# Kernel tuning notes

Hardware: AMD Instinct MI355X
Metric: run time of the kernel (lower is better)

The kernel has to match this reference:

```python
import jax, jax.numpy as jnp
import numpy as np

M, N, EMB, H, ENC, T = 4096, 256, 64, 128, 128, 100


def _lstm_dir(x, Wih, Whh, b, h0, c0):
    # x: (T, M, E); PyTorch LSTM gate order i, f, g, o
    def step(carry, xt):
        h, c = carry
        g = xt @ Wih + h @ Whh + b
        i, f, gg, o = jnp.split(g, 4, axis=-1)
        c = jax.nn.sigmoid(f) * c + jax.nn.sigmoid(i) * jnp.tanh(gg)
        h = jax.nn.sigmoid(o) * jnp.tanh(c)
        return (h, c), h
    _, hs = jax.lax.scan(step, (h0, c0), x)
    return hs  # (T, M, H)


def setup_inputs() -> dict:
    key = jax.random.key(0)
    ks = jax.random.split(key, 14)
    rn = lambda k, sh, s: jax.random.normal(k, sh, jnp.float32) * s
    return {
        "lane_features": jax.random.normal(ks[0], (M, 600), jnp.float32),
        "obs_encoding": jax.random.normal(ks[1], (N, 128), jnp.float32),
        "embed_W": rn(ks[2], (4, EMB), 0.5),
        "embed_b": jnp.zeros((EMB,), jnp.float32),
        "attn_W": rn(ks[3], (128, 100), 0.09),
        "attn_b": jnp.zeros((100,), jnp.float32),
        "Wih_f": rn(ks[4], (EMB, 4 * H), 0.08),
        "Whh_f": rn(ks[5], (H, 4 * H), 0.08),
        "b_f": jnp.zeros((4 * H,), jnp.float32),
        "Wih_b": rn(ks[6], (EMB, 4 * H), 0.08),
        "Whh_b": rn(ks[7], (H, 4 * H), 0.08),
        "b_b": jnp.zeros((4 * H,), jnp.float32),
        "h0": rn(ks[8], (2, 1, H), 0.1),
        "c0": rn(ks[9], (2, 1, H), 0.1),
        "enc_W": rn(ks[10], (8 * H, ENC), 0.03),
        "enc_b": jnp.zeros((ENC,), jnp.float32),
        "same_obs_mask": jax.random.randint(ks[11], (M, 1), 0, N, jnp.int32),
    }


def reference(lane_features, obs_encoding, embed_W, embed_b, attn_W, attn_b,
              Wih_f, Whh_f, b_f, Wih_b, Whh_b, b_b, h0, c0, enc_W, enc_b,
              same_obs_mask):
    Mloc = lane_features.shape[0]
    E = embed_W.shape[1]
    Hh = Whh_f.shape[0]
    # last 400 features -> 100 timesteps x 4 features, then embed + relu
    feat = lane_features[:, -400:].reshape(Mloc * 100, 4)
    lane_embed = jax.nn.relu(feat @ embed_W + embed_b).reshape(Mloc, 100, E)
    # per-obstacle attention over the 100 lane points
    scores = jax.nn.softmax(jax.nn.relu(obs_encoding @ attn_W + attn_b), axis=1)  # (N, 100)
    # the original per-obs_id scatter loop == a single gather by obstacle id
    att = scores[same_obs_mask[:, 0]]  # (M, 100)
    x = jnp.transpose(lane_embed, (1, 0, 2))  # (T, M, E)
    h0f = jnp.broadcast_to(h0[0], (Mloc, Hh)); c0f = jnp.broadcast_to(c0[0], (Mloc, Hh))
    h0b = jnp.broadcast_to(h0[1], (Mloc, Hh)); c0b = jnp.broadcast_to(c0[1], (Mloc, Hh))
    hs_f = _lstm_dir(x, Wih_f, Whh_f, b_f, h0f, c0f)
    hs_b = _lstm_dir(x[::-1], Wih_b, Whh_b, b_b, h0b, c0b)[::-1]
    ls = jnp.transpose(jnp.concatenate([hs_f, hs_b], axis=-1), (1, 0, 2))  # (M, T, 2H)
    front = ls[:, 0, :]
    back = ls[:, -1, :]
    mx = jnp.max(ls, axis=1)
    attn_states = jnp.sum(ls * att[:, :, None], axis=1)
    out = jnp.concatenate([front, back, mx, attn_states], axis=1)  # (M, 8H)
    return jax.nn.relu(out @ enc_W + enc_b)
```

## Files before the change

### kernel.cpp

```cpp
#include <hip/hip_runtime.h>
#include <hip/hip_bf16.h>

#define MROWS 4096
#define TSTEPS 100
#define EMB 64
#define HID 128
#define GATES 512
#define KTOT 192
#define ROWS_PB 32
#define SROW 200

typedef _Float16 half8 __attribute__((ext_vector_type(8)));
typedef float f32x4 __attribute__((ext_vector_type(4)));

#define LOG2E  1.44269504f
#define LOG2E2 2.88539008f

__device__ __forceinline__ float rcpf(float x) { return __builtin_amdgcn_rcpf(x); }
__device__ __forceinline__ float ex2(float x) { return __builtin_amdgcn_exp2f(x); }

__global__ void prep_kernel(const float* __restrict__ obs,
                            const float* __restrict__ attn_W,
                            const float* __restrict__ attn_b,
                            float* __restrict__ scores,
                            const float* __restrict__ enc_W,
                            _Float16* __restrict__ frag) {
    const int tid = threadIdx.x;
    if (blockIdx.x < 256) {
        const int row = blockIdx.x;
        __shared__ float obs_s[128];
        __shared__ float red[128];

        if (tid < 128) obs_s[tid] = obs[row * 128 + tid];
        __syncthreads();

        float s = -1e30f;
        if (tid < 100) {
            float a = attn_b[tid];
            #pragma unroll 4
            for (int k = 0; k < 128; k++) a += obs_s[k] * attn_W[k * 100 + tid];
            s = fmaxf(a, 0.f);
        }
        if (tid < 128) red[tid] = s;
        __syncthreads();
        for (int off = 64; off > 0; off >>= 1) {
            if (tid < off) red[tid] = fmaxf(red[tid], red[tid + off]);
            __syncthreads();
        }
        const float m = red[0];
        __syncthreads();
        const float e = (tid < 100) ? __expf(s - m) : 0.f;
        if (tid < 128) red[tid] = e;
        __syncthreads();
        for (int off = 64; off > 0; off >>= 1) {
            if (tid < off) red[tid] += red[tid + off];
            __syncthreads();
        }
        const float inv = __fdividef(1.f, red[0]);
        if (tid < 100) scores[row * 100 + tid] = e * inv;
    } else {
        const int pb = blockIdx.x - 256;
        const int pair = pb * 16 + (tid >> 4);
        const int tile = pair >> 5;
        const int it   = pair & 31;
        const int sub  = tid & 15;
        #pragma unroll
        for (int li = 0; li < 4; li++) {
            const int l = sub * 4 + li;
            const int c = tile * 16 + (l & 15);
            const int kbase = it * 32 + (l >> 4) * 8;
            half8 v;
            #pragma unroll
            for (int j = 0; j < 8; j++) v[j] = (_Float16)enc_W[(kbase + j) * 128 + c];
            *(half8*)(frag + (((long)(tile * 32 + it)) * 64 + l) * 8) = v;
        }
    }
}

__launch_bounds__(512, 2)
__global__ void lstm_kernel(const float* __restrict__ lane_features,
                            const float* __restrict__ embed_W,
                            const float* __restrict__ embed_b,
                            const float* __restrict__ Wih_f,
                            const float* __restrict__ Whh_f,
                            const float* __restrict__ b_f,
                            const float* __restrict__ Wih_b,
                            const float* __restrict__ Whh_b,
                            const float* __restrict__ b_b,
                            const float* __restrict__ h0,
                            const float* __restrict__ c0,
                            const int*   __restrict__ mask,
                            const float* __restrict__ scores,
                            _Float16* __restrict__ out_feat) {
    const int blk = blockIdx.x;
    const int d = blk >> 7;
    const int rowbase = (blk & 127) * ROWS_PB;
    const int tid = threadIdx.x;
    const int wave = tid >> 6;
    const int lane = tid & 63;
    const int lane16 = lane & 15;
    const int quad = lane >> 4;

    const float* Wih = d ? Wih_b : Wih_f;
    const float* Whh = d ? Whh_b : Whh_f;
    const float* bia = d ? b_b : b_f;

    __shared__ __attribute__((aligned(16))) _Float16 panel[2][ROWS_PB][SROW];
    __shared__ float att_s[ROWS_PB][100];

    const int erow = tid >> 4;
    const int cc = (tid & 15) * 4;
    float ew_r[4][4], eb_r[4];
    #pragma unroll
    for (int j = 0; j < 4; j++) {
        #pragma unroll
        for (int jj = 0; jj < 4; jj++) ew_r[j][jj] = embed_W[j * EMB + cc + jj];
    }
    #pragma unroll
    for (int jj = 0; jj < 4; jj++) eb_r[jj] = embed_b[cc + jj];

    {
        const int r = tid >> 4, tcol = tid & 15;
        const int mr = mask[rowbase + r];
        for (int t = tcol; t < 100; t += 16) att_s[r][t] = scores[mr * 100 + t];
    }

    const int unitg = wave * 16 + lane16;
    half8 Bf[24];
    #pragma unroll
    for (int ct = 0; ct < 4; ct++) {
        const float scale = (ct == 2) ? LOG2E2 : LOG2E;
        const int col = ct * 128 + unitg;
        #pragma unroll
        for (int ki = 0; ki < 6; ki++) {
            half8 b;
            #pragma unroll
            for (int j = 0; j < 8; j++) {
                const int kk = ki * 32 + quad * 8 + j;
                const float w = (kk < EMB) ? Wih[kk * GATES + col]
                                           : Whh[(kk - EMB) * GATES + col];
                b[j] = (_Float16)(w * scale);
            }
            Bf[ct * 6 + ki] = b;
        }
    }
    float bgate[4];
    #pragma unroll
    for (int ct = 0; ct < 4; ct++)
        bgate[ct] = bia[ct * 128 + unitg] * ((ct == 2) ? LOG2E2 : LOG2E);

    float cst[8], mx[8], as[8], h0s[8], hl[8];
    const float cinit = c0[d * 128 + unitg];
    #pragma unroll
    for (int p = 0; p < 8; p++) {
        cst[p] = cinit; mx[p] = -1e30f; as[p] = 0.f; h0s[p] = 0.f; hl[p] = 0.f;
    }

    for (int idx = tid; idx < ROWS_PB * HID; idx += 512) {
        const int r = idx >> 7, u = idx & 127;
        panel[0][r][EMB + u] = (_Float16)h0[d * 128 + u];
    }

    {
        const int t0 = d ? (TSTEPS - 1) : 0;
        const float4 fv = *(const float4*)(lane_features + (long)(rowbase + erow) * 600 + 200 + 4 * t0);
        #pragma unroll
        for (int jj = 0; jj < 4; jj++) {
            float e = eb_r[jj] + fv.x * ew_r[0][jj] + fv.y * ew_r[1][jj]
                               + fv.z * ew_r[2][jj] + fv.w * ew_r[3][jj];
            panel[0][erow][cc + jj] = (_Float16)fmaxf(e, 0.f);
        }
    }
    __syncthreads();

    for (int s = 0; s < TSTEPS; s++) {
        const int p = s & 1;
        const int t = d ? (TSTEPS - 1 - s) : s;

        float4 fv;
        if (s < TSTEPS - 1) {
            const int tn = d ? (TSTEPS - 2 - s) : (s + 1);
            fv = *(const float4*)(lane_features + (long)(rowbase + erow) * 600 + 200 + 4 * tn);
        }

        float aw[8];
        #pragma unroll
        for (int pp = 0; pp < 8; pp++) {
            const int row_local = (pp >> 2) * 16 + quad * 4 + (pp & 3);
            aw[pp] = att_s[row_local][t];
        }

        f32x4 acc[2][4];
        #pragma unroll
        for (int rt = 0; rt < 2; rt++)
            #pragma unroll
            for (int ct = 0; ct < 4; ct++) {
                const float bg = bgate[ct];
                acc[rt][ct] = (f32x4){bg, bg, bg, bg};
            }

        #pragma unroll
        for (int ki = 0; ki < 6; ki++) {
            const half8 a0 = *(const half8*)&panel[p][lane16][ki * 32 + quad * 8];
            const half8 a1 = *(const half8*)&panel[p][16 + lane16][ki * 32 + quad * 8];
            #pragma unroll
            for (int ct = 0; ct < 4; ct++) {
                acc[0][ct] = __builtin_amdgcn_mfma_f32_16x16x32_f16(a0, Bf[ct * 6 + ki], acc[0][ct], 0, 0, 0);
                acc[1][ct] = __builtin_amdgcn_mfma_f32_16x16x32_f16(a1, Bf[ct * 6 + ki], acc[1][ct], 0, 0, 0);
            }
        }

        #pragma unroll
        for (int rt = 0; rt < 2; rt++) {
            #pragma unroll
            for (int r = 0; r < 4; r++) {
                const int pp = rt * 4 + r;
                const int row_local = rt * 16 + quad * 4 + r;
                const float gi = acc[rt][0][r];
                const float gf = acc[rt][1][r];
                const float gg = fminf(acc[rt][2][r], 80.f);
                const float go = acc[rt][3][r];
                const float Ei = ex2(-gi);
                const float Ef = ex2(-gf);
                const float Eg = ex2(gg);
                const float Eo = ex2(-go);
                const float sf = rcpf(1.f + Ef);
                const float r1 = rcpf((1.f + Ei) * (Eg + 1.f));
                const float cn = sf * cst[pp] + (Eg - 1.f) * r1;
                const float Ec = ex2(fminf(cn * LOG2E2, 80.f));
                const float r2 = rcpf((1.f + Eo) * (Ec + 1.f));
                const float h = (Ec - 1.f) * r2;
                cst[pp] = cn;
                hl[pp] = h;
                mx[pp] = fmaxf(mx[pp], h);
                as[pp] = fmaf(aw[pp], h, as[pp]);
                panel[1 - p][row_local][EMB + unitg] = (_Float16)h;
            }
        }
        if (s == 0) {
            #pragma unroll
            for (int pp = 0; pp < 8; pp++) h0s[pp] = hl[pp];
        }

        if (s < TSTEPS - 1) {
            float e0 = eb_r[0] + fv.x * ew_r[0][0] + fv.y * ew_r[1][0] + fv.z * ew_r[2][0] + fv.w * ew_r[3][0];
            float e1 = eb_r[1] + fv.x * ew_r[0][1] + fv.y * ew_r[1][1] + fv.z * ew_r[2][1] + fv.w * ew_r[3][1];
            float e2 = eb_r[2] + fv.x * ew_r[0][2] + fv.y * ew_r[1][2] + fv.z * ew_r[2][2] + fv.w * ew_r[3][2];
            float e3 = eb_r[3] + fv.x * ew_r[0][3] + fv.y * ew_r[1][3] + fv.z * ew_r[2][3] + fv.w * ew_r[3][3];
            panel[1 - p][erow][cc]     = (_Float16)fmaxf(e0, 0.f);
            panel[1 - p][erow][cc + 1] = (_Float16)fmaxf(e1, 0.f);
            panel[1 - p][erow][cc + 2] = (_Float16)fmaxf(e2, 0.f);
            panel[1 - p][erow][cc + 3] = (_Float16)fmaxf(e3, 0.f);
        }
        __syncthreads();
    }

    #pragma unroll
    for (int pp = 0; pp < 8; pp++) {
        const int row_local = (pp >> 2) * 16 + quad * 4 + (pp & 3);
        const long ro = (long)(rowbase + row_local) * 1024;
        const int cu = d * 128 + unitg;
        const float fr = d ? hl[pp] : h0s[pp];
        const float bk = d ? h0s[pp] : hl[pp];
        out_feat[ro + cu]       = (_Float16)fr;
        out_feat[ro + 256 + cu] = (_Float16)bk;
        out_feat[ro + 512 + cu] = (_Float16)mx[pp];
        out_feat[ro + 768 + cu] = (_Float16)as[pp];
    }
}

__launch_bounds__(256, 2)
__global__ void enc_kernel(const _Float16* __restrict__ out_feat,
                           const _Float16* __restrict__ frag,
                           const float* __restrict__ enc_b,
                           float* __restrict__ out) {
    const int rb = blockIdx.x * 16;
    const int tid = threadIdx.x;
    const int wave = tid >> 6;
    const int lane = tid & 63;
    const int lane16 = lane & 15;
    const int quad = lane >> 4;

    __shared__ __attribute__((aligned(16))) _Float16 A16[16][1032];

    #pragma unroll
    for (int i = 0; i < 8; i++) {
        const int u = tid + i * 256;
        const int row = u >> 7, kc = u & 127;
        *(half8*)&A16[row][kc * 8] = *(const half8*)(out_feat + (long)(rb + row) * 1024 + kc * 8);
    }
    __syncthreads();

    const int col0 = wave * 32 + lane16;
    f32x4 acc0 = {0.f, 0.f, 0.f, 0.f}, acc1 = {0.f, 0.f, 0.f, 0.f};

    const _Float16* f0 = frag + ((long)(2 * wave) * 32 * 64) * 8 + lane * 8;
    const _Float16* f1 = frag + ((long)(2 * wave + 1) * 32 * 64) * 8 + lane * 8;

    #pragma unroll 4
    for (int it = 0; it < 32; it++) {
        const half8 a  = *(const half8*)&A16[lane16][it * 32 + quad * 8];
        const half8 b0 = *(const half8*)(f0 + (long)it * 64 * 8);
        const half8 b1 = *(const half8*)(f1 + (long)it * 64 * 8);
        acc0 = __builtin_amdgcn_mfma_f32_16x16x32_f16(a, b0, acc0, 0, 0, 0);
        acc1 = __builtin_amdgcn_mfma_f32_16x16x32_f16(a, b1, acc1, 0, 0, 0);
    }

    const float bb0 = enc_b[col0], bb1 = enc_b[col0 + 16];
    #pragma unroll
    for (int r = 0; r < 4; r++) {
        const int row = rb + quad * 4 + r;
        out[(long)row * 128 + col0]      = fmaxf(acc0[r] + bb0, 0.f);
        out[(long)row * 128 + col0 + 16] = fmaxf(acc1[r] + bb1, 0.f);
    }
}

extern "C" void kernel_launch(void* const* d_in, const int* in_sizes, int n_in,
                              void* d_out, int out_size, void* d_ws, size_t ws_size,
                              hipStream_t stream) {
    const float* lane_features = (const float*)d_in[0];
    const float* obs_encoding  = (const float*)d_in[1];
    const float* embed_W = (const float*)d_in[2];
    const float* embed_b = (const float*)d_in[3];
    const float* attn_W  = (const float*)d_in[4];
    const float* attn_b  = (const float*)d_in[5];
    const float* Wih_f   = (const float*)d_in[6];
    const float* Whh_f   = (const float*)d_in[7];
    const float* b_f     = (const float*)d_in[8];
    const float* Wih_b   = (const float*)d_in[9];
    const float* Whh_b   = (const float*)d_in[10];
    const float* b_b     = (const float*)d_in[11];
    const float* h0      = (const float*)d_in[12];
    const float* c0      = (const float*)d_in[13];
    const float* enc_W   = (const float*)d_in[14];
    const float* enc_b   = (const float*)d_in[15];
    const int*   mask    = (const int*)d_in[16];

    float*     scores   = (float*)d_ws;
    _Float16*  frag     = (_Float16*)((char*)d_ws + (128 << 10));
    _Float16*  out_feat = (_Float16*)((char*)d_ws + (512 << 10));
    float*     out      = (float*)d_out;

    prep_kernel<<<272, 256, 0, stream>>>(obs_encoding, attn_W, attn_b, scores,
                                         enc_W, frag);
    lstm_kernel<<<256, 512, 0, stream>>>(lane_features, embed_W, embed_b,
                                         Wih_f, Whh_f, b_f, Wih_b, Whh_b, b_b,
                                         h0, c0, mask, scores, out_feat);
    enc_kernel<<<256, 256, 0, stream>>>(out_feat, frag, enc_b, out);
}
```

Before: 299.6 us.

## Fuse encoder GEMM partials into LSTM kernel epilogue, add small reduce kernel

Each LSTM block now writes its pooled features (front/back/max/attention) into shared memory and multiplies them by its direction's slice of the encoder weights with MFMA. It stores per-direction fp32 partial sums instead of the fp16 feature matrix. A small elementwise kernel then adds the two direction partials, applies the bias and ReLU. This removes the global round trip of the 4096x1024 fp16 intermediate and the heavier encoder GEMM kernel. In exchange, the LSTM kernel gets a longer epilogue and writes 2x4096x128 fp32 partials.

```diff
diff --git a/kernel.cpp b/kernel.cpp
--- a/kernel.cpp
+++ b/kernel.cpp
@@ -9,6 +9,7 @@
 #define KTOT 192
 #define ROWS_PB 32
 #define SROW 200
+#define PSTR 520
 
 typedef _Float16 half8 __attribute__((ext_vector_type(8)));
 typedef float f32x4 __attribute__((ext_vector_type(4)));
@@ -91,7 +92,8 @@
                             const float* __restrict__ c0,
                             const int*   __restrict__ mask,
                             const float* __restrict__ scores,
-                            _Float16* __restrict__ out_feat) {
+                            const _Float16* __restrict__ frag,
+                            float* __restrict__ pacc) {
     const int blk = blockIdx.x;
     const int d = blk >> 7;
     const int rowbase = (blk & 127) * ROWS_PB;
@@ -105,8 +107,10 @@
     const float* Whh = d ? Whh_b : Whh_f;
     const float* bia = d ? b_b : b_f;
 
-    __shared__ __attribute__((aligned(16))) _Float16 panel[2][ROWS_PB][SROW];
-    __shared__ float att_s[ROWS_PB][100];
+    __shared__ __attribute__((aligned(16))) char smem[38400];
+    auto panel = (_Float16 (*)[ROWS_PB][SROW])smem;
+    float (*att_s)[100] = (float (*)[100])(smem + 25600);
+    _Float16* pool = (_Float16*)smem;
 
     const int erow = tid >> 4;
     const int cc = (tid & 15) * 4;
@@ -258,61 +262,48 @@
     #pragma unroll
     for (int pp = 0; pp < 8; pp++) {
         const int row_local = (pp >> 2) * 16 + quad * 4 + (pp & 3);
-        const long ro = (long)(rowbase + row_local) * 1024;
-        const int cu = d * 128 + unitg;
         const float fr = d ? hl[pp] : h0s[pp];
         const float bk = d ? h0s[pp] : hl[pp];
-        out_feat[ro + cu]       = (_Float16)fr;
-        out_feat[ro + 256 + cu] = (_Float16)bk;
-        out_feat[ro + 512 + cu] = (_Float16)mx[pp];
-        out_feat[ro + 768 + cu] = (_Float16)as[pp];
+        pool[row_local * PSTR + 0 * 128 + unitg] = (_Float16)fr;
+        pool[row_local * PSTR + 1 * 128 + unitg] = (_Float16)bk;
+        pool[row_local * PSTR + 2 * 128 + unitg] = (_Float16)mx[pp];
+        pool[row_local * PSTR + 3 * 128 + unitg] = (_Float16)as[pp];
+    }
+    __syncthreads();
+
+    f32x4 cacc0 = {0.f, 0.f, 0.f, 0.f}, cacc1 = {0.f, 0.f, 0.f, 0.f};
+    const _Float16* fbase = frag + ((long)wave * 32) * 64 * 8 + lane * 8;
+    #pragma unroll
+    for (int lc = 0; lc < 16; lc++) {
+        const int seg = lc >> 2, c = lc & 3;
+        const int itg = seg * 8 + d * 4 + c;
+        const half8 b  = *(const half8*)(fbase + (long)itg * 64 * 8);
+        const half8 a0 = *(const half8*)&pool[lane16 * PSTR + lc * 32 + quad * 8];
+        const half8 a1 = *(const half8*)&pool[(16 + lane16) * PSTR + lc * 32 + quad * 8];
+        cacc0 = __builtin_amdgcn_mfma_f32_16x16x32_f16(a0, b, cacc0, 0, 0, 0);
+        cacc1 = __builtin_amdgcn_mfma_f32_16x16x32_f16(a1, b, cacc1, 0, 0, 0);
+    }
+    float* pacc_d = pacc + (long)d * MROWS * 128;
+    #pragma unroll
+    for (int r = 0; r < 4; r++) {
+        pacc_d[(long)(rowbase + quad * 4 + r) * 128 + wave * 16 + lane16]      = cacc0[r];
+        pacc_d[(long)(rowbase + 16 + quad * 4 + r) * 128 + wave * 16 + lane16] = cacc1[r];
     }
 }
 
-__launch_bounds__(256, 2)
-__global__ void enc_kernel(const _Float16* __restrict__ out_feat,
-                           const _Float16* __restrict__ frag,
-                           const float* __restrict__ enc_b,
-                           float* __restrict__ out) {
-    const int rb = blockIdx.x * 16;
-    const int tid = threadIdx.x;
-    const int wave = tid >> 6;
-    const int lane = tid & 63;
-    const int lane16 = lane & 15;
-    const int quad = lane >> 4;
-
-    __shared__ __attribute__((aligned(16))) _Float16 A16[16][1032];
-
-    #pragma unroll
-    for (int i = 0; i < 8; i++) {
-        const int u = tid + i * 256;
-        const int row = u >> 7, kc = u & 127;
-        *(half8*)&A16[row][kc * 8] = *(const half8*)(out_feat + (long)(rb + row) * 1024 + kc * 8);
-    }
-    __syncthreads();
-
-    const int col0 = wave * 32 + lane16;
-    f32x4 acc0 = {0.f, 0.f, 0.f, 0.f}, acc1 = {0.f, 0.f, 0.f, 0.f};
-
-    const _Float16* f0 = frag + ((long)(2 * wave) * 32 * 64) * 8 + lane * 8;
-    const _Float16* f1 = frag + ((long)(2 * wave + 1) * 32 * 64) * 8 + lane * 8;
-
-    #pragma unroll 4
-    for (int it = 0; it < 32; it++) {
-        const half8 a  = *(const half8*)&A16[lane16][it * 32 + quad * 8];
-        const half8 b0 = *(const half8*)(f0 + (long)it * 64 * 8);
-        const half8 b1 = *(const half8*)(f1 + (long)it * 64 * 8);
-        acc0 = __builtin_amdgcn_mfma_f32_16x16x32_f16(a, b0, acc0, 0, 0, 0);
-        acc1 = __builtin_amdgcn_mfma_f32_16x16x32_f16(a, b1, acc1, 0, 0, 0);
-    }
-
-    const float bb0 = enc_b[col0], bb1 = enc_b[col0 + 16];
-    #pragma unroll
-    for (int r = 0; r < 4; r++) {
-        const int row = rb + quad * 4 + r;
-        out[(long)row * 128 + col0]      = fmaxf(acc0[r] + bb0, 0.f);
-        out[(long)row * 128 + col0 + 16] = fmaxf(acc1[r] + bb1, 0.f);
-    }
+__global__ void final_kernel(const float* __restrict__ pacc,
+                             const float* __restrict__ enc_b,
+                             float* __restrict__ out) {
+    const int idx = (blockIdx.x * 256 + threadIdx.x) * 4;
+    const float4 a = *(const float4*)(pacc + idx);
+    const float4 b = *(const float4*)(pacc + (long)MROWS * 128 + idx);
+    const float4 bb = *(const float4*)(enc_b + (idx & 127));
+    float4 o;
+    o.x = fmaxf(a.x + b.x + bb.x, 0.f);
+    o.y = fmaxf(a.y + b.y + bb.y, 0.f);
+    o.z = fmaxf(a.z + b.z + bb.z, 0.f);
+    o.w = fmaxf(a.w + b.w + bb.w, 0.f);
+    *(float4*)(out + idx) = o;
 }
 
 extern "C" void kernel_launch(void* const* d_in, const int* in_sizes, int n_in,
@@ -336,15 +327,15 @@
     const float* enc_b   = (const float*)d_in[15];
     const int*   mask    = (const int*)d_in[16];
 
-    float*     scores   = (float*)d_ws;
-    _Float16*  frag     = (_Float16*)((char*)d_ws + (128 << 10));
-    _Float16*  out_feat = (_Float16*)((char*)d_ws + (512 << 10));
-    float*     out      = (float*)d_out;
+    float*     scores = (float*)d_ws;
+    _Float16*  frag   = (_Float16*)((char*)d_ws + (128 << 10));
+    float*     pacc   = (float*)((char*)d_ws + (512 << 10));
+    float*     out    = (float*)d_out;
 
     prep_kernel<<<272, 256, 0, stream>>>(obs_encoding, attn_W, attn_b, scores,
                                          enc_W, frag);
     lstm_kernel<<<256, 512, 0, stream>>>(lane_features, embed_W, embed_b,
                                          Wih_f, Whh_f, b_f, Wih_b, Whh_b, b_b,
-                                         h0, c0, mask, scores, out_feat);
-    enc_kernel<<<256, 256, 0, stream>>>(out_feat, frag, enc_b, out);
+                                         h0, c0, mask, scores, frag, pacc);
+    final_kernel<<<512, 256, 0, stream>>>(pacc, enc_b, out);
 }
```

Measured after the change: 292.4 us. 2.4% less time.
